# Performance work log

Measured on AMD Instinct MI355X. Metric: run time of the kernel, lower is better.

The kernel has to match this reference:

```python
import jax, jax.numpy as jnp
import numpy as np

B, S, D = 2, 2048, 1024
H = 16
HD = D // H  # 64
EPS = 1e-5


def setup_inputs() -> dict:
    key = jax.random.key(0)
    ks = jax.random.split(key, 9)
    s = 1.0 / np.sqrt(D)
    return {
        "x": jax.random.normal(ks[0], (B, S, D), jnp.float32),
        "Wq": jax.random.normal(ks[1], (D, D), jnp.float32) * s,
        "bq": jnp.zeros((D,), jnp.float32),
        "Wk": jax.random.normal(ks[2], (D, D), jnp.float32) * s,
        "bk": jnp.zeros((D,), jnp.float32),
        "Wv": jax.random.normal(ks[3], (D, D), jnp.float32) * s,
        "bv": jnp.zeros((D,), jnp.float32),
        "Wp": jax.random.normal(ks[4], (D, D), jnp.float32) * s,
        "bp": jnp.zeros((D,), jnp.float32),
        "gamma": jnp.ones((D,), jnp.float32),
        "beta": jnp.zeros((D,), jnp.float32),
    }


def reference(x, Wq, bq, Wk, bk, Wv, bv, Wp, bp, gamma, beta):
    # QKV projections -> [B, H, S, HD]
    def split_heads(t):
        return t.reshape(B, S, H, HD).transpose(0, 2, 1, 3)

    q = split_heads(x @ Wq + bq)
    k = split_heads(x @ Wk + bk)
    v = split_heads(x @ Wv + bv)

    scores = jnp.einsum('bhqd,bhkd->bhqk', q, k) / np.sqrt(HD).astype(jnp.float32)
    attn = jax.nn.softmax(scores, axis=-1)  # dropout in eval mode = identity
    out = jnp.einsum('bhqk,bhkd->bhqd', attn, v)
    out = out.transpose(0, 2, 1, 3).reshape(B, S, D)
    out = out @ Wp + bp  # dropout identity

    # residual + LayerNorm over last dim
    y = x + out
    mu = jnp.mean(y, axis=-1, keepdims=True)
    var = jnp.mean((y - mu) ** 2, axis=-1, keepdims=True)
    return (y - mu) / jnp.sqrt(var + EPS) * gamma + beta
```

## Files before the change

### kernel.cpp

```cpp
#include <hip/hip_runtime.h>

#define DI __device__ __forceinline__

typedef __bf16 bf16;
typedef __bf16 bf16x8 __attribute__((ext_vector_type(8)));
typedef __bf16 bf16x4 __attribute__((ext_vector_type(4)));
typedef float  f32x4  __attribute__((ext_vector_type(4)));

DI void async_copy16(const void* g, void* s) {
  __builtin_amdgcn_global_load_lds(
      (__attribute__((address_space(1))) unsigned int*)(void*)g,
      (__attribute__((address_space(3))) unsigned int*)s,
      16, 0, 0);
}

DI f32x4 mfma16(bf16x8 a, bf16x8 b, f32x4 c) {
  return __builtin_amdgcn_mfma_f32_16x16x32_bf16(a, b, c, 0, 0, 0);
}

__global__ __launch_bounds__(256) void prep(const float* __restrict__ x,
                                            const float* __restrict__ Wq,
                                            const float* __restrict__ Wk,
                                            const float* __restrict__ Wv,
                                            const float* __restrict__ Wp,
                                            bf16* __restrict__ xb,
                                            bf16* __restrict__ Wt) {
  if (blockIdx.z == 4) {
    int blk = blockIdx.y * 32 + blockIdx.x;
    int base = blk * 4096 + threadIdx.x * 4;
#pragma unroll
    for (int j = 0; j < 4; ++j) {
      float4 v = *(const float4*)&x[base + j * 1024];
      bf16x4 o;
      o[0] = (bf16)v.x; o[1] = (bf16)v.y; o[2] = (bf16)v.z; o[3] = (bf16)v.w;
      *(bf16x4*)&xb[base + j * 1024] = o;
    }
    return;
  }
  __shared__ float tile[32][33];
  const float* W = (blockIdx.z == 0) ? Wq : (blockIdx.z == 1) ? Wk
                 : (blockIdx.z == 2) ? Wv : Wp;
  int n0 = blockIdx.x * 32, k0 = blockIdx.y * 32;
  int tx = threadIdx.x & 31, ty = threadIdx.x >> 5;
#pragma unroll
  for (int i = 0; i < 4; ++i)
    tile[ty + i * 8][tx] = W[(k0 + ty + i * 8) * 1024 + n0 + tx];
  __syncthreads();
#pragma unroll
  for (int i = 0; i < 4; ++i)
    Wt[((int)blockIdx.z * 1024 + n0 + ty + i * 8) * 1024 + k0 + tx] =
        (bf16)tile[tx][ty + i * 8];
}

template <int MODE, int MT, int NT>
__global__ __launch_bounds__(256, 3) void gemm_bt(
    const bf16* __restrict__ A, const bf16* __restrict__ Bt,
    const float* __restrict__ bias0, const float* __restrict__ bias1,
    const float* __restrict__ bias2, bf16* __restrict__ Qo,
    bf16* __restrict__ Ko, bf16* __restrict__ Vo, bf16* __restrict__ Po) {
  constexpr int MW = MT / 2, NW = NT / 2;
  constexpr int MI = MW / 16, NI = NW / 16;
  const int tid = threadIdx.x;
  const int w = tid >> 6, lane = tid & 63, quad = lane >> 4, m16 = lane & 15;
  const int m0 = blockIdx.x * MT, n0 = blockIdx.y * NT;
  const int mw = (w >> 1) * MW, nw = (w & 1) * NW;
  const int sw = m16 & 7;

  __shared__ __align__(16) bf16 As[MT * 64];
  __shared__ __align__(16) bf16 Bs[NT * 64];

  f32x4 acc[MI][NI];
#pragma unroll
  for (int i = 0; i < MI; ++i)
#pragma unroll
    for (int j = 0; j < NI; ++j)
#pragma unroll
      for (int r = 0; r < 4; ++r) acc[i][j][r] = 0.0f;

  for (int k0 = 0; k0 < 1024; k0 += 64) {
    __syncthreads();
#pragma unroll
    for (int i = 0; i < MT / 32; ++i) {
      int lin = i * 256 + tid;
      int row = lin >> 3, p = lin & 7;
      async_copy16(&A[(m0 + row) * 1024 + k0 + ((p ^ (row & 7)) << 3)],
                   &As[(i * 256 + w * 64) * 8]);
    }
#pragma unroll
    for (int i = 0; i < NT / 32; ++i) {
      int lin = i * 256 + tid;
      int row = lin >> 3, p = lin & 7;
      async_copy16(&Bt[(n0 + row) * 1024 + k0 + ((p ^ (row & 7)) << 3)],
                   &Bs[(i * 256 + w * 64) * 8]);
    }
    __syncthreads();

#pragma unroll
    for (int kk = 0; kk < 2; ++kk) {
      const int pos = ((kk * 4 + quad) ^ sw) << 3;
      bf16x8 af[MI], bg[NI];
#pragma unroll
      for (int i = 0; i < MI; ++i)
        af[i] = *(const bf16x8*)&As[(mw + i * 16 + m16) * 64 + pos];
#pragma unroll
      for (int j = 0; j < NI; ++j)
        bg[j] = *(const bf16x8*)&Bs[(nw + j * 16 + m16) * 64 + pos];
#pragma unroll
      for (int i = 0; i < MI; ++i)
#pragma unroll
        for (int j = 0; j < NI; ++j) acc[i][j] = mfma16(af[i], bg[j], acc[i][j]);
    }
  }

  const float SC = 0.18033688011112042f;
#pragma unroll
  for (int i = 0; i < MI; ++i) {
#pragma unroll
    for (int j = 0; j < NI; ++j) {
      int np = n0 + nw + j * 16 + m16;
      if (MODE == 0) {
        int which = np >> 10, n = np & 1023;
        float bias = (which == 0) ? bias0[n] : (which == 1) ? bias1[n] : bias2[n];
        int h = n >> 6, hd = n & 63;
        if (which == 2) {
          bf16x4 pv;
          int m = m0 + mw + i * 16 + quad * 4;
          int b = m >> 11, s = m & 2047;
#pragma unroll
          for (int r = 0; r < 4; ++r) pv[r] = (bf16)(acc[i][j][r] + bias);
          *(bf16x4*)&Vo[((b * 16 + h) * 64 + hd) * 2048 + s] = pv;
        } else {
#pragma unroll
          for (int r = 0; r < 4; ++r) {
            int m = m0 + mw + i * 16 + quad * 4 + r;
            int b = m >> 11, s = m & 2047;
            float v = acc[i][j][r] + bias;
            if (which == 0)
              Qo[((b * 16 + h) * 2048 + s) * 64 + hd] = (bf16)(v * SC);
            else
              Ko[((b * 16 + h) * 2048 + s) * 64 + hd] = (bf16)v;
          }
        }
      } else {
        float bias = bias0[np];
#pragma unroll
        for (int r = 0; r < 4; ++r) {
          int m = m0 + mw + i * 16 + quad * 4 + r;
          Po[m * 1024 + np] = (bf16)(acc[i][j][r] + bias);
        }
      }
    }
  }
}

__global__ __launch_bounds__(256, 2) void flash_kernel(const bf16* __restrict__ Q,
                                                       const bf16* __restrict__ K,
                                                       const bf16* __restrict__ Vt,
                                                       bf16* __restrict__ attn) {
  const int S = 2048;
  const int tid = threadIdx.x;
  const int w = tid >> 6, lane = tid & 63, quad = lane >> 4, m16 = lane & 15;
  const int bh = blockIdx.x, b = bh >> 4, h = bh & 15;
  const int qb = blockIdx.y * 128;
  const bf16* Qh = Q + bh * S * 64;
  const bf16* Kh = K + bh * S * 64;
  const bf16* Vh = Vt + bh * 64 * S;

  __shared__ __align__(16) bf16 Ks[2][64 * 64];
  __shared__ __align__(16) bf16 Vs[2][64 * 64];
  __shared__ __align__(16) bf16 Ps[4][16 * 72];

  bf16x8 qf[2][2];
#pragma unroll
  for (int mi = 0; mi < 2; ++mi)
#pragma unroll
    for (int kk = 0; kk < 2; ++kk)
      qf[mi][kk] = *(const bf16x8*)&Qh[(qb + w * 32 + mi * 16 + m16) * 64 +
                                       kk * 32 + quad * 8];

  bf16x8 ones;
#pragma unroll
  for (int j = 0; j < 8; ++j) ones[j] = (bf16)1.0f;

  f32x4 o[2][4];
  f32x4 lacc[2];
#pragma unroll
  for (int mi = 0; mi < 2; ++mi) {
#pragma unroll
    for (int dt = 0; dt < 4; ++dt)
#pragma unroll
      for (int r = 0; r < 4; ++r) o[mi][dt][r] = 0.0f;
#pragma unroll
    for (int r = 0; r < 4; ++r) lacc[mi][r] = 0.0f;
  }

  auto stage = [&](int kb, int buf) {
#pragma unroll
    for (int i = 0; i < 2; ++i) {
      int lin = i * 256 + tid;
      int row = lin >> 3, g = lin & 7;
      async_copy16(&Kh[(kb + row) * 64 + ((g ^ (row & 7)) << 3)],
                   &Ks[buf][(i * 256 + w * 64) * 8]);
      async_copy16(&Vh[row * 2048 + kb + ((g ^ (row & 7)) << 3)],
                   &Vs[buf][(i * 256 + w * 64) * 8]);
    }
  };

  stage(0, 0);

  for (int t = 0; t < 32; ++t) {
    const int cur = t & 1;
    if (t < 31) {
      stage((t + 1) * 64, cur ^ 1);
      asm volatile("s_waitcnt vmcnt(4)" ::: "memory");
    } else {
      asm volatile("s_waitcnt vmcnt(0)" ::: "memory");
    }
    asm volatile("s_barrier" ::: "memory");

    bf16x8 kf[4][2], vf[4][2];
#pragma unroll
    for (int nt = 0; nt < 4; ++nt)
#pragma unroll
      for (int kk = 0; kk < 2; ++kk) {
        int row = nt * 16 + m16;
        int pos = (kk * 4 + quad) ^ (row & 7);
        kf[nt][kk] = *(const bf16x8*)&Ks[cur][row * 64 + pos * 8];
        vf[nt][kk] = *(const bf16x8*)&Vs[cur][row * 64 + pos * 8];
      }
    asm volatile("s_waitcnt lgkmcnt(0)" ::: "memory");
    asm volatile("s_barrier" ::: "memory");

    bf16* Pw = &Ps[w][0];
#pragma unroll
    for (int mi = 0; mi < 2; ++mi) {
      f32x4 sacc[4];
#pragma unroll
      for (int nt = 0; nt < 4; ++nt)
#pragma unroll
        for (int r = 0; r < 4; ++r) sacc[nt][r] = 0.0f;
#pragma unroll
      for (int nt = 0; nt < 4; ++nt)
#pragma unroll
        for (int kk = 0; kk < 2; ++kk)
          sacc[nt] = mfma16(kf[nt][kk], qf[mi][kk], sacc[nt]);

#pragma unroll
      for (int nt = 0; nt < 4; ++nt) {
        bf16x4 p4;
#pragma unroll
        for (int r = 0; r < 4; ++r)
          p4[r] = (bf16)__builtin_amdgcn_exp2f(sacc[nt][r]);
        *(bf16x4*)&Pw[m16 * 72 + nt * 16 + quad * 4] = p4;
      }
      asm volatile("s_waitcnt lgkmcnt(0)" ::: "memory");

      bf16x8 pf[2];
#pragma unroll
      for (int kk = 0; kk < 2; ++kk)
        pf[kk] = *(const bf16x8*)&Pw[m16 * 72 + kk * 32 + quad * 8];

#pragma unroll
      for (int kk = 0; kk < 2; ++kk) lacc[mi] = mfma16(pf[kk], ones, lacc[mi]);

#pragma unroll
      for (int dt = 0; dt < 4; ++dt)
#pragma unroll
        for (int kk = 0; kk < 2; ++kk)
          o[mi][dt] = mfma16(pf[kk], vf[dt][kk], o[mi][dt]);
    }
  }

#pragma unroll
  for (int mi = 0; mi < 2; ++mi) {
    f32x4 inv;
#pragma unroll
    for (int r = 0; r < 4; ++r) inv[r] = 1.0f / lacc[mi][r];
#pragma unroll
    for (int dt = 0; dt < 4; ++dt)
#pragma unroll
      for (int r = 0; r < 4; ++r) {
        int s = qb + w * 32 + mi * 16 + quad * 4 + r;
        int col = h * 64 + dt * 16 + m16;
        attn[(b * 2048 + s) * 1024 + col] = (bf16)(o[mi][dt][r] * inv[r]);
      }
  }
}

__global__ __launch_bounds__(256) void ln_kernel(const float* __restrict__ x,
                                                 const bf16* __restrict__ pj,
                                                 const float* __restrict__ gamma,
                                                 const float* __restrict__ beta,
                                                 float* __restrict__ out) {
  int row = blockIdx.x, t = threadIdx.x;
  int base = row * 1024 + t * 4;
  float4 xv = *(const float4*)&x[base];
  bf16x4 pv4 = *(const bf16x4*)&pj[base];
  float y0 = xv.x + (float)pv4[0], y1 = xv.y + (float)pv4[1];
  float y2 = xv.z + (float)pv4[2], y3 = xv.w + (float)pv4[3];
  float s = y0 + y1 + y2 + y3;
  float ss = y0 * y0 + y1 * y1 + y2 * y2 + y3 * y3;
  for (int m = 1; m < 64; m <<= 1) {
    s += __shfl_xor(s, m);
    ss += __shfl_xor(ss, m);
  }
  __shared__ float sred[8];
  int w = t >> 6;
  if ((t & 63) == 0) { sred[w * 2] = s; sred[w * 2 + 1] = ss; }
  __syncthreads();
  s = sred[0] + sred[2] + sred[4] + sred[6];
  ss = sred[1] + sred[3] + sred[5] + sred[7];
  float mean = s * (1.0f / 1024.0f);
  float var = ss * (1.0f / 1024.0f) - mean * mean;
  float rstd = rsqrtf(var + 1e-5f);
  float4 gv = *(const float4*)&gamma[t * 4];
  float4 bv = *(const float4*)&beta[t * 4];
  float4 ov;
  ov.x = (y0 - mean) * rstd * gv.x + bv.x;
  ov.y = (y1 - mean) * rstd * gv.y + bv.y;
  ov.z = (y2 - mean) * rstd * gv.z + bv.z;
  ov.w = (y3 - mean) * rstd * gv.w + bv.w;
  *(float4*)&out[base] = ov;
}


extern "C" void kernel_launch(void* const* d_in, const int* in_sizes, int n_in,
                              void* d_out, int out_size, void* d_ws, size_t ws_size,
                              hipStream_t stream) {
  const float* x = (const float*)d_in[0];
  const float* Wq = (const float*)d_in[1];
  const float* bq = (const float*)d_in[2];
  const float* Wk = (const float*)d_in[3];
  const float* bk = (const float*)d_in[4];
  const float* Wv = (const float*)d_in[5];
  const float* bv = (const float*)d_in[6];
  const float* Wp = (const float*)d_in[7];
  const float* bp = (const float*)d_in[8];
  const float* gamma = (const float*)d_in[9];
  const float* beta = (const float*)d_in[10];
  float* out = (float*)d_out;

  char* ws = (char*)d_ws;
  bf16* xb = (bf16*)(ws);
  bf16* Wtb = (bf16*)(ws + (8u << 20));
  bf16* Qb = (bf16*)(ws + (16u << 20));
  bf16* Kb = (bf16*)(ws + (24u << 20));
  bf16* Vtb = (bf16*)(ws + (32u << 20));
  bf16* proj = (bf16*)(ws + (16u << 20));
  bf16* attn = xb;

  prep<<<dim3(32, 32, 5), 256, 0, stream>>>(x, Wq, Wk, Wv, Wp, xb, Wtb);
  gemm_bt<0, 128, 128><<<dim3(32, 24), 256, 0, stream>>>(
      xb, Wtb, bq, bk, bv, Qb, Kb, Vtb, nullptr);
  flash_kernel<<<dim3(32, 16), 256, 0, stream>>>(Qb, Kb, Vtb, attn);
  gemm_bt<1, 64, 128><<<dim3(64, 8), 256, 0, stream>>>(
      attn, Wtb + 3072 * 1024, bp, nullptr, nullptr, nullptr, nullptr, nullptr,
      proj);
  ln_kernel<<<4096, 256, 0, stream>>>(x, proj, gamma, beta, out);
}
```

Before: 191.6 us.

## Use 8 waves per flash block with 16 query rows per wave

```diff
diff --git a/kernel.cpp b/kernel.cpp
--- a/kernel.cpp
+++ b/kernel.cpp
@@ -153,7 +153,7 @@
   }
 }
 
-__global__ __launch_bounds__(256, 2) void flash_kernel(const bf16* __restrict__ Q,
+__global__ __launch_bounds__(512, 4) void flash_kernel(const bf16* __restrict__ Q,
                                                        const bf16* __restrict__ K,
                                                        const bf16* __restrict__ Vt,
                                                        bf16* __restrict__ attn) {
@@ -168,42 +168,32 @@
 
   __shared__ __align__(16) bf16 Ks[2][64 * 64];
   __shared__ __align__(16) bf16 Vs[2][64 * 64];
-  __shared__ __align__(16) bf16 Ps[4][16 * 72];
-
-  bf16x8 qf[2][2];
-#pragma unroll
-  for (int mi = 0; mi < 2; ++mi)
-#pragma unroll
-    for (int kk = 0; kk < 2; ++kk)
-      qf[mi][kk] = *(const bf16x8*)&Qh[(qb + w * 32 + mi * 16 + m16) * 64 +
-                                       kk * 32 + quad * 8];
+  __shared__ __align__(16) bf16 Ps[8][16 * 72];
+
+  bf16x8 qf[2];
+#pragma unroll
+  for (int kk = 0; kk < 2; ++kk)
+    qf[kk] = *(const bf16x8*)&Qh[(qb + w * 16 + m16) * 64 + kk * 32 + quad * 8];
 
   bf16x8 ones;
 #pragma unroll
   for (int j = 0; j < 8; ++j) ones[j] = (bf16)1.0f;
 
-  f32x4 o[2][4];
-  f32x4 lacc[2];
-#pragma unroll
-  for (int mi = 0; mi < 2; ++mi) {
-#pragma unroll
-    for (int dt = 0; dt < 4; ++dt)
-#pragma unroll
-      for (int r = 0; r < 4; ++r) o[mi][dt][r] = 0.0f;
-#pragma unroll
-    for (int r = 0; r < 4; ++r) lacc[mi][r] = 0.0f;
-  }
+  f32x4 o[4];
+  f32x4 lacc;
+#pragma unroll
+  for (int dt = 0; dt < 4; ++dt)
+#pragma unroll
+    for (int r = 0; r < 4; ++r) o[dt][r] = 0.0f;
+#pragma unroll
+  for (int r = 0; r < 4; ++r) lacc[r] = 0.0f;
 
   auto stage = [&](int kb, int buf) {
-#pragma unroll
-    for (int i = 0; i < 2; ++i) {
-      int lin = i * 256 + tid;
-      int row = lin >> 3, g = lin & 7;
-      async_copy16(&Kh[(kb + row) * 64 + ((g ^ (row & 7)) << 3)],
-                   &Ks[buf][(i * 256 + w * 64) * 8]);
-      async_copy16(&Vh[row * 2048 + kb + ((g ^ (row & 7)) << 3)],
-                   &Vs[buf][(i * 256 + w * 64) * 8]);
-    }
+    int row = tid >> 3, g = tid & 7;
+    async_copy16(&Kh[(kb + row) * 64 + ((g ^ (row & 7)) << 3)],
+                 &Ks[buf][w * 512]);
+    async_copy16(&Vh[row * 2048 + kb + ((g ^ (row & 7)) << 3)],
+                 &Vs[buf][w * 512]);
   };
 
   stage(0, 0);
@@ -212,7 +202,7 @@
     const int cur = t & 1;
     if (t < 31) {
       stage((t + 1) * 64, cur ^ 1);
-      asm volatile("s_waitcnt vmcnt(4)" ::: "memory");
+      asm volatile("s_waitcnt vmcnt(2)" ::: "memory");
     } else {
       asm volatile("s_waitcnt vmcnt(0)" ::: "memory");
     }
@@ -231,60 +221,54 @@
     asm volatile("s_waitcnt lgkmcnt(0)" ::: "memory");
     asm volatile("s_barrier" ::: "memory");
 
+    f32x4 sacc[4];
+#pragma unroll
+    for (int nt = 0; nt < 4; ++nt)
+#pragma unroll
+      for (int r = 0; r < 4; ++r) sacc[nt][r] = 0.0f;
+#pragma unroll
+    for (int nt = 0; nt < 4; ++nt)
+#pragma unroll
+      for (int kk = 0; kk < 2; ++kk)
+        sacc[nt] = mfma16(kf[nt][kk], qf[kk], sacc[nt]);
+
     bf16* Pw = &Ps[w][0];
 #pragma unroll
-    for (int mi = 0; mi < 2; ++mi) {
-      f32x4 sacc[4];
-#pragma unroll
-      for (int nt = 0; nt < 4; ++nt)
-#pragma unroll
-        for (int r = 0; r < 4; ++r) sacc[nt][r] = 0.0f;
-#pragma unroll
-      for (int nt = 0; nt < 4; ++nt)
-#pragma unroll
-        for (int kk = 0; kk < 2; ++kk)
-          sacc[nt] = mfma16(kf[nt][kk], qf[mi][kk], sacc[nt]);
-
-#pragma unroll
-      for (int nt = 0; nt < 4; ++nt) {
-        bf16x4 p4;
-#pragma unroll
-        for (int r = 0; r < 4; ++r)
-          p4[r] = (bf16)__builtin_amdgcn_exp2f(sacc[nt][r]);
-        *(bf16x4*)&Pw[m16 * 72 + nt * 16 + quad * 4] = p4;
-      }
-      asm volatile("s_waitcnt lgkmcnt(0)" ::: "memory");
-
-      bf16x8 pf[2];
+    for (int nt = 0; nt < 4; ++nt) {
+      bf16x4 p4;
+#pragma unroll
+      for (int r = 0; r < 4; ++r)
+        p4[r] = (bf16)__builtin_amdgcn_exp2f(sacc[nt][r]);
+      *(bf16x4*)&Pw[m16 * 72 + nt * 16 + quad * 4] = p4;
+    }
+    asm volatile("s_waitcnt lgkmcnt(0)" ::: "memory");
+
+    bf16x8 pf[2];
+#pragma unroll
+    for (int kk = 0; kk < 2; ++kk)
+      pf[kk] = *(const bf16x8*)&Pw[m16 * 72 + kk * 32 + quad * 8];
+
+#pragma unroll
+    for (int kk = 0; kk < 2; ++kk) lacc = mfma16(pf[kk], ones, lacc);
+
+#pragma unroll
+    for (int dt = 0; dt < 4; ++dt)
 #pragma unroll
       for (int kk = 0; kk < 2; ++kk)
-        pf[kk] = *(const bf16x8*)&Pw[m16 * 72 + kk * 32 + quad * 8];
-
-#pragma unroll
-      for (int kk = 0; kk < 2; ++kk) lacc[mi] = mfma16(pf[kk], ones, lacc[mi]);
-
-#pragma unroll
-      for (int dt = 0; dt < 4; ++dt)
-#pragma unroll
-        for (int kk = 0; kk < 2; ++kk)
-          o[mi][dt] = mfma16(pf[kk], vf[dt][kk], o[mi][dt]);
-    }
-  }
-
-#pragma unroll
-  for (int mi = 0; mi < 2; ++mi) {
-    f32x4 inv;
-#pragma unroll
-    for (int r = 0; r < 4; ++r) inv[r] = 1.0f / lacc[mi][r];
-#pragma unroll
-    for (int dt = 0; dt < 4; ++dt)
-#pragma unroll
-      for (int r = 0; r < 4; ++r) {
-        int s = qb + w * 32 + mi * 16 + quad * 4 + r;
-        int col = h * 64 + dt * 16 + m16;
-        attn[(b * 2048 + s) * 1024 + col] = (bf16)(o[mi][dt][r] * inv[r]);
-      }
-  }
+        o[dt] = mfma16(pf[kk], vf[dt][kk], o[dt]);
+  }
+
+  f32x4 inv;
+#pragma unroll
+  for (int r = 0; r < 4; ++r) inv[r] = 1.0f / lacc[r];
+#pragma unroll
+  for (int dt = 0; dt < 4; ++dt)
+#pragma unroll
+    for (int r = 0; r < 4; ++r) {
+      int s = qb + w * 16 + quad * 4 + r;
+      int col = h * 64 + dt * 16 + m16;
+      attn[(b * 2048 + s) * 1024 + col] = (bf16)(o[dt][r] * inv[r]);
+    }
 }
 
 __global__ __launch_bounds__(256) void ln_kernel(const float* __restrict__ x,
@@ -352,7 +336,7 @@
   prep<<<dim3(32, 32, 5), 256, 0, stream>>>(x, Wq, Wk, Wv, Wp, xb, Wtb);
   gemm_bt<0, 128, 128><<<dim3(32, 24), 256, 0, stream>>>(
       xb, Wtb, bq, bk, bv, Qb, Kb, Vtb, nullptr);
-  flash_kernel<<<dim3(32, 16), 256, 0, stream>>>(Qb, Kb, Vtb, attn);
+  flash_kernel<<<dim3(32, 16), 512, 0, stream>>>(Qb, Kb, Vtb, attn);
   gemm_bt<1, 64, 128><<<dim3(64, 8), 256, 0, stream>>>(
       attn, Wtb + 3072 * 1024, bp, nullptr, nullptr, nullptr, nullptr, nullptr,
       proj);
```

After: 188.8 us. Within noise of the previous version (-1.4%).
